# Kernel optimization log

Hardware: AMD Instinct MI355X
Metric: run time of the kernel (lower is better)

The kernel has to match this reference:

```python
import jax, jax.numpy as jnp
import numpy as np

N = 50000
E = 1600000
IN_C = 512
HID = 64
OUT_C = 64
HEADS = 2
K = 2
NEG_SLOPE = 0.2


def setup_inputs() -> dict:
    key = jax.random.key(0)
    ks = jax.random.split(key, 9)
    x = jax.random.normal(ks[0], (N, IN_C), dtype=jnp.float32)
    edge_index = jax.random.randint(ks[1], (2, E), 0, N, dtype=jnp.int64)
    edge_attr = jax.random.uniform(ks[2], (E,), dtype=jnp.float32)
    # SGConv linear (glorot-ish init)
    W_sg = jax.random.normal(ks[3], (IN_C, HID), dtype=jnp.float32) / np.sqrt(IN_C)
    b_sg = jnp.zeros((HID,), dtype=jnp.float32)
    # GATConv: lin (no bias), attention vectors, output bias (concat=False -> size OUT_C)
    W_gat = jax.random.normal(ks[4], (HID, HEADS * OUT_C), dtype=jnp.float32) / np.sqrt(HID)
    att_src = jax.random.normal(ks[5], (HEADS, OUT_C), dtype=jnp.float32) / np.sqrt(OUT_C)
    att_dst = jax.random.normal(ks[6], (HEADS, OUT_C), dtype=jnp.float32) / np.sqrt(OUT_C)
    b_gat = jnp.zeros((OUT_C,), dtype=jnp.float32)
    return {"x": x, "edge_index": edge_index, "edge_attr": edge_attr,
            "W_sg": W_sg, "b_sg": b_sg, "W_gat": W_gat,
            "att_src": att_src, "att_dst": att_dst, "b_gat": b_gat}


def reference(x, edge_index, edge_attr, W_sg, b_sg, W_gat, att_src, att_dst, b_gat):
    n = x.shape[0]
    src, dst = edge_index[0], edge_index[1]
    # add self-loops (weight 1) once; reused by SGConv (gcn_norm) and GAT
    loop = jnp.arange(n, dtype=src.dtype)
    src2 = jnp.concatenate([src, loop])
    dst2 = jnp.concatenate([dst, loop])
    ew = jnp.concatenate([edge_attr, jnp.ones((n,), x.dtype)])

    # ---- SGConv: K hops of D^-1/2 A D^-1/2, then linear ----
    deg = jax.ops.segment_sum(ew, dst2, num_segments=n)
    dinv = jnp.where(deg > 0, jax.lax.rsqrt(deg), 0.0)
    norm = dinv[src2] * ew * dinv[dst2]  # [E+N]
    h = x
    for _ in range(K):
        h = jax.ops.segment_sum(norm[:, None] * h[src2], dst2, num_segments=n)
    h = h @ W_sg + b_sg  # [N, HID]

    # activation (SELU); dropout is identity in eval mode
    h = jax.nn.selu(h)

    # ---- GATConv (heads, concat=False -> mean over heads) ----
    g = (h @ W_gat).reshape(n, HEADS, OUT_C)  # [N, H, C]
    a_src = jnp.einsum('nhc,hc->nh', g, att_src)  # [N, H]
    a_dst = jnp.einsum('nhc,hc->nh', g, att_dst)
    e = jax.nn.leaky_relu(a_src[src2] + a_dst[dst2], NEG_SLOPE)  # [E+N, H]
    # per-destination softmax (numerically stable)
    emax = jax.ops.segment_max(e, dst2, num_segments=n)
    emax = jnp.where(jnp.isfinite(emax), emax, 0.0)
    ee = jnp.exp(e - emax[dst2])
    denom = jax.ops.segment_sum(ee, dst2, num_segments=n)
    alpha = ee / jnp.maximum(denom[dst2], 1e-16)  # [E+N, H]
    out = jax.ops.segment_sum(alpha[:, :, None] * g[src2], dst2, num_segments=n)  # [N, H, C]
    return out.mean(axis=1) + b_gat  # [N, OUT_C]
```

## Files before the change

kernel.cpp:

```cpp
#include <hip/hip_runtime.h>
#include <hip/hip_fp16.h>
#include <math.h>

#define N_NODES 50000
#define N_EDGES 1600000
#define IN_CH 512
#define HID 64
#define OUTC 64
#define NEG_SLOPE 0.2f
#define EA_SCALE 131072.0f
#define PCAP 128
#define SLOTS 96

typedef __attribute__((ext_vector_type(8))) short bf16x8;
typedef __attribute__((ext_vector_type(4))) float f32x4;

__device__ __forceinline__ unsigned bf16r(float f) {
    unsigned b = __float_as_uint(f);
    return (b + 0x7FFFu + ((b >> 16) & 1u)) >> 16;
}

__device__ __forceinline__ void gload16(const void* g, void* l) {
    __builtin_amdgcn_global_load_lds(
        (const __attribute__((address_space(1))) void*)g,
        (__attribute__((address_space(3))) void*)l, 16, 0, 0);
}

__global__ void k_wsplit(const float* __restrict__ W, short* __restrict__ Wfrag) {
    int idx = blockIdx.x * 256 + threadIdx.x;
    if (idx >= IN_CH * HID) return;
    int k = idx >> 6, c = idx & 63;
    float wv = W[idx];
    unsigned h = bf16r(wv);
    float res = wv - __uint_as_float(h << 16);
    unsigned l = bf16r(res);
    int kstep = k >> 5, cb = c >> 4;
    int lane = (c & 15) | (((k >> 3) & 3) << 4);
    int j = k & 7;
    int base = ((kstep * 4 + cb) * 2) * 512 + lane * 8 + j;
    Wfrag[base] = (short)h;
    Wfrag[base + 512] = (short)l;
}

#define G1R 64
#define G1KC 64
__global__ __launch_bounds__(256) void k_gemm_hist(const float* __restrict__ x,
                                                   const short* __restrict__ Wfrag,
                                                   __half* __restrict__ p,
                                                   const int* __restrict__ src,
                                                   const int* __restrict__ dst,
                                                   const float* __restrict__ ea,
                                                   unsigned* __restrict__ deg32,
                                                   int* __restrict__ edges4) {
    __shared__ float xs[2][G1R][G1KC];
    int tid = threadIdx.x;
    int bid = blockIdx.x;

    if (bid & 1) {
        int e0 = (bid >> 1) * 2048;
        int e1 = e0 + 2048; if (e1 > N_EDGES) e1 = N_EDGES;
        for (int e = e0 + tid; e < e1; e += 256) {
            int d = dst[e];
            float w = ea[e];
            unsigned pack = (1u << 24) | (unsigned)(w * EA_SCALE);
            unsigned old = atomicAdd(&deg32[d], pack);
            int rank = (int)(old >> 24);
            if (rank < SLOTS)
                edges4[d * SLOTS + rank] =
                    (src[e] << 16) | (int)__half_as_ushort(__float2half_rn(w));
        }
        return;
    }

    int lane = tid & 63, wv = tid >> 6;
    int r0 = (bid >> 1) * G1R;
    f32x4 acc0 = {0.f, 0.f, 0.f, 0.f};
    f32x4 acc1 = {0.f, 0.f, 0.f, 0.f};
    f32x4 acc2 = {0.f, 0.f, 0.f, 0.f};
    f32x4 acc3 = {0.f, 0.f, 0.f, 0.f};

    auto stage = [&](int b, int k0) {
#pragma unroll
        for (int it = 0; it < 4; it++) {
            int rowbase = it * 16 + wv * 4;
            int row = rowbase + (lane >> 4);
            int gr = r0 + row; if (gr > N_NODES - 1) gr = N_NODES - 1;
            int col = ((lane & 15) ^ (row & 7)) << 2;
            gload16(x + (size_t)gr * IN_CH + k0 + col, &xs[b][rowbase][0]);
        }
    };

    stage(0, 0);
    asm volatile("s_waitcnt vmcnt(0)" ::: "memory");
    __syncthreads();

    int cur = 0;
    int arow = wv * 16 + (lane & 15);
    const char* xsbase = (const char*)&xs[0][0][0];
    for (int k0 = 0; k0 < IN_CH; k0 += G1KC) {
        if (k0 + G1KC < IN_CH) stage(cur ^ 1, k0 + G1KC);
#pragma unroll
        for (int kk = 0; kk < 2; kk++) {
            int ks = (k0 >> 5) + kk;
            const short* wb = Wfrag + ks * 4096 + (lane << 3);
            bf16x8 bh0 = *(const bf16x8*)(wb);
            bf16x8 bl0 = *(const bf16x8*)(wb + 512);
            bf16x8 bh1 = *(const bf16x8*)(wb + 1024);
            bf16x8 bl1 = *(const bf16x8*)(wb + 1536);
            bf16x8 bh2 = *(const bf16x8*)(wb + 2048);
            bf16x8 bl2 = *(const bf16x8*)(wb + 2560);
            bf16x8 bh3 = *(const bf16x8*)(wb + 3072);
            bf16x8 bl3 = *(const bf16x8*)(wb + 3584);
            int c16 = kk * 8 + ((lane >> 4) << 1);
            size_t rb = (size_t)cur * (G1R * G1KC * 4) + (size_t)arow * (G1KC * 4);
            float4 xa = *(const float4*)(xsbase + rb + (((c16    ) ^ (arow & 7)) << 4));
            float4 xb = *(const float4*)(xsbase + rb + (((c16 + 1) ^ (arow & 7)) << 4));
            float xv[8] = {xa.x, xa.y, xa.z, xa.w, xb.x, xb.y, xb.z, xb.w};
            bf16x8 ah, al;
#pragma unroll
            for (int j = 0; j < 8; j++) {
                unsigned b = __float_as_uint(xv[j]);
                float res = xv[j] - __uint_as_float(b & 0xFFFF0000u);
                ah[j] = (short)(b >> 16);
                al[j] = (short)(__float_as_uint(res) >> 16);
            }
            acc0 = __builtin_amdgcn_mfma_f32_16x16x32_bf16(ah, bh0, acc0, 0, 0, 0);
            acc0 = __builtin_amdgcn_mfma_f32_16x16x32_bf16(ah, bl0, acc0, 0, 0, 0);
            acc0 = __builtin_amdgcn_mfma_f32_16x16x32_bf16(al, bh0, acc0, 0, 0, 0);
            acc1 = __builtin_amdgcn_mfma_f32_16x16x32_bf16(ah, bh1, acc1, 0, 0, 0);
            acc1 = __builtin_amdgcn_mfma_f32_16x16x32_bf16(ah, bl1, acc1, 0, 0, 0);
            acc1 = __builtin_amdgcn_mfma_f32_16x16x32_bf16(al, bh1, acc1, 0, 0, 0);
            acc2 = __builtin_amdgcn_mfma_f32_16x16x32_bf16(ah, bh2, acc2, 0, 0, 0);
            acc2 = __builtin_amdgcn_mfma_f32_16x16x32_bf16(ah, bl2, acc2, 0, 0, 0);
            acc2 = __builtin_amdgcn_mfma_f32_16x16x32_bf16(al, bh2, acc2, 0, 0, 0);
            acc3 = __builtin_amdgcn_mfma_f32_16x16x32_bf16(ah, bh3, acc3, 0, 0, 0);
            acc3 = __builtin_amdgcn_mfma_f32_16x16x32_bf16(ah, bl3, acc3, 0, 0, 0);
            acc3 = __builtin_amdgcn_mfma_f32_16x16x32_bf16(al, bh3, acc3, 0, 0, 0);
        }
        asm volatile("s_waitcnt vmcnt(0)" ::: "memory");
        __syncthreads();
        cur ^= 1;
    }
    int crow = r0 + wv * 16 + ((lane >> 4) << 2);
    int ccol = lane & 15;
#pragma unroll
    for (int r = 0; r < 4; r++) {
        int gr = crow + r;
        if (gr < N_NODES) {
            p[(unsigned)gr * HID + ccol]      = __float2half(acc0[r]);
            p[(unsigned)gr * HID + 16 + ccol] = __float2half(acc1[r]);
            p[(unsigned)gr * HID + 32 + ccol] = __float2half(acc2[r]);
            p[(unsigned)gr * HID + 48 + ccol] = __float2half(acc3[r]);
        }
    }
}

__global__ void k_hscale(unsigned* __restrict__ h2, const unsigned* __restrict__ deg32,
                         float* __restrict__ dinv) {
    int idx = blockIdx.x * 256 + threadIdx.x;
    if (idx >= N_NODES * 32) return;
    int v = idx >> 5;
    float dv = rsqrtf(1.0f + (float)(deg32[v] & 0xFFFFFFu) * (1.0f / EA_SCALE));
    if ((idx & 31) == 0) dinv[v] = dv;
    unsigned u = h2[idx];
    float2 f = __half22float2(*(__half2*)&u);
    __half2 r = __floats2half2_rn(f.x * dv, f.y * dv);
    h2[idx] = *(unsigned*)&r;
}

__global__ __launch_bounds__(256) void k_hop(const uint2* __restrict__ hin4,
                                             const unsigned* __restrict__ deg32,
                                             const int* __restrict__ edges4,
                                             const float* __restrict__ dinv,
                                             uint2* __restrict__ hout4,
                                             int pw) {
    __shared__ float4 part[2][16];
    int tid = threadIdx.x;
    int w = tid >> 6, lane = tid & 63;
    int slot = w >> 1, half = w & 1;
    int cl = lane & 15, es = lane >> 4;
    int v = blockIdx.x * 2 + slot;
    int cnt = (int)(deg32[v] >> 24);
    if (cnt > SLOTS) cnt = SLOTS;
    int beg = v * SLOTS, end = beg + cnt;
    int mid = beg + (cnt >> 1);
    int lo = half ? mid : beg;
    int hi = half ? end : mid;
    float a0 = 0.f, a1 = 0.f, a2 = 0.f, a3 = 0.f;
    float b0 = 0.f, b1 = 0.f, b2 = 0.f, b3 = 0.f;
    if (!half && !es) {
        uint2 u = hin4[(unsigned)v * 16 + cl];
        float2 f0 = __half22float2(*(__half2*)&u.x);
        float2 f1 = __half22float2(*(__half2*)&u.y);
        a0 = f0.x; a1 = f0.y; a2 = f1.x; a3 = f1.y;
    }
    int i = lo;
    for (; i + 8 <= hi; i += 8) {
        int r0 = edges4[i + es];
        int r1 = edges4[i + 4 + es];
        uint2 g0 = hin4[(((unsigned)r0 >> 16) << 4) + cl];
        uint2 g1 = hin4[(((unsigned)r1 >> 16) << 4) + cl];
        float w0 = __half2float(__ushort_as_half((unsigned short)(r0 & 0xFFFF)));
        float w1 = __half2float(__ushort_as_half((unsigned short)(r1 & 0xFFFF)));
        float2 g0a = __half22float2(*(__half2*)&g0.x);
        float2 g0b = __half22float2(*(__half2*)&g0.y);
        float2 g1a = __half22float2(*(__half2*)&g1.x);
        float2 g1b = __half22float2(*(__half2*)&g1.y);
        a0 += w0 * g0a.x; a1 += w0 * g0a.y; a2 += w0 * g0b.x; a3 += w0 * g0b.y;
        b0 += w1 * g1a.x; b1 += w1 * g1a.y; b2 += w1 * g1b.x; b3 += w1 * g1b.y;
    }
    for (; i + es < hi; i += 4) {
        int r0 = edges4[i + es];
        uint2 g0 = hin4[(((unsigned)r0 >> 16) << 4) + cl];
        float w0 = __half2float(__ushort_as_half((unsigned short)(r0 & 0xFFFF)));
        float2 g0a = __half22float2(*(__half2*)&g0.x);
        float2 g0b = __half22float2(*(__half2*)&g0.y);
        a0 += w0 * g0a.x; a1 += w0 * g0a.y; a2 += w0 * g0b.x; a3 += w0 * g0b.y;
    }
    a0 += b0; a1 += b1; a2 += b2; a3 += b3;
    a0 += __shfl_xor(a0, 16); a1 += __shfl_xor(a1, 16);
    a2 += __shfl_xor(a2, 16); a3 += __shfl_xor(a3, 16);
    a0 += __shfl_xor(a0, 32); a1 += __shfl_xor(a1, 32);
    a2 += __shfl_xor(a2, 32); a3 += __shfl_xor(a3, 32);
    if (half && lane < 16) part[slot][cl] = make_float4(a0, a1, a2, a3);
    __syncthreads();
    if (!half && lane < 16) {
        float dv = dinv[v];
        float sc = (pw == 2) ? dv * dv : dv;
        float4 pp = part[slot][cl];
        __half2 h0 = __floats2half2_rn(sc * (a0 + pp.x), sc * (a1 + pp.y));
        __half2 h1 = __floats2half2_rn(sc * (a2 + pp.z), sc * (a3 + pp.w));
        hout4[(unsigned)v * 16 + cl] = make_uint2(*(unsigned*)&h0, *(unsigned*)&h1);
    }
}

#define G2_ROWS 32
__global__ __launch_bounds__(256) void k_act_gemm2(const __half* __restrict__ h2,
                                                   const float* __restrict__ bsg,
                                                   const float* __restrict__ Wg,
                                                   const float* __restrict__ att_s,
                                                   const float* __restrict__ att_d,
                                                   uint2* __restrict__ g4h,
                                                   float2* __restrict__ asrc2,
                                                   float4* __restrict__ admm) {
    __shared__ float hs[G2_ROWS][HID];
    int tid = threadIdx.x;
    int wave = tid >> 6, lane = tid & 63;
    int r0 = blockIdx.x * G2_ROWS;
    int rbase = wave * 8;

    const float SC = 1.0507009873554805f, AL = 1.6732632423543772f;
    {
        int row = tid >> 3, c0 = (tid & 7) * 8;
        int r = r0 + row;
        float vals[8];
        if (r < N_NODES) {
            uint4 raw = *(const uint4*)(h2 + (unsigned)r * HID + c0);
            float2 f0 = __half22float2(*(__half2*)&raw.x);
            float2 f1 = __half22float2(*(__half2*)&raw.y);
            float2 f2 = __half22float2(*(__half2*)&raw.z);
            float2 f3 = __half22float2(*(__half2*)&raw.w);
            vals[0] = f0.x; vals[1] = f0.y; vals[2] = f1.x; vals[3] = f1.y;
            vals[4] = f2.x; vals[5] = f2.y; vals[6] = f3.x; vals[7] = f3.y;
        } else {
#pragma unroll
            for (int j = 0; j < 8; j++) vals[j] = 0.f;
        }
#pragma unroll
        for (int j = 0; j < 8; j++) {
            float hv = vals[j] + bsg[c0 + j];
            hv = (hv > 0.f) ? SC * hv : SC * AL * (__expf(hv) - 1.f);
            hs[row][c0 + j] = hv;
        }
    }
    __syncthreads();

    float accx[8], accy[8];
#pragma unroll
    for (int j = 0; j < 8; j++) { accx[j] = 0.f; accy[j] = 0.f; }
#pragma unroll 2
    for (int k = 0; k < HID; k++) {
        float w0 = Wg[(size_t)k * 128 + lane];
        float w1 = Wg[(size_t)k * 128 + 64 + lane];
#pragma unroll
        for (int j = 0; j < 8; j++) {
            float hk = hs[rbase + j][k];
            accx[j] += hk * w0;
            accy[j] += hk * w1;
        }
    }
    float ats0 = att_s[lane], ats1 = att_s[64 + lane];
    float atd0 = att_d[lane], atd1 = att_d[64 + lane];
#pragma unroll
    for (int j = 0; j < 8; j++) {
        int v = r0 + rbase + j;
        if (v >= N_NODES) break;
        __half2 gp = __floats2half2_rn(accx[j], accy[j]);
        unsigned gpu = *(unsigned*)&gp;
        unsigned other = (unsigned)__shfl_xor((int)gpu, 1);
        if (!(lane & 1)) g4h[(unsigned)v * 32 + (lane >> 1)] = make_uint2(gpu, other);
        float s0 = accx[j] * ats0, s1 = accy[j] * ats1;
        float d0 = accx[j] * atd0, d1 = accy[j] * atd1;
#pragma unroll
        for (int o = 32; o > 0; o >>= 1) {
            s0 += __shfl_xor(s0, o);
            s1 += __shfl_xor(s1, o);
            d0 += __shfl_xor(d0, o);
            d1 += __shfl_xor(d1, o);
        }
        if (lane == 0) {
            asrc2[v] = make_float2(s0, s1);
            float m0 = s0 + d0; m0 = (m0 > 0.f) ? m0 : NEG_SLOPE * m0;
            float m1 = s1 + d1; m1 = (m1 > 0.f) ? m1 : NEG_SLOPE * m1;
            admm[v] = make_float4(d0, d1, m0, m1);
        }
    }
}

__global__ __launch_bounds__(256) void k_gat(const uint2* __restrict__ g4h,
                                             const float2* __restrict__ asrc2,
                                             const float4* __restrict__ admm,
                                             const unsigned* __restrict__ deg32,
                                             const int* __restrict__ edges4,
                                             const float* __restrict__ bgat,
                                             float* __restrict__ out) {
    __shared__ int4 pbuf[2][2][PCAP];
    __shared__ float4 pacc[2][32];
    __shared__ float2 pden[2][32];
    int tid = threadIdx.x;
    int w = tid >> 6, lane = tid & 63;
    int slot = w >> 1, half = w & 1;
    int cl = lane & 31, es = lane >> 5;
    int v = blockIdx.x * 2 + slot;
    float4 am = admm[v];
    int cnt = (int)(deg32[v] >> 24);
    if (cnt > SLOTS) cnt = SLOTS;
    int beg = v * SLOTS, end = beg + cnt;
    int mid = beg + (cnt >> 1);
    int lo = half ? mid : beg;
    int hi = half ? end : mid;
    int n = hi - lo;

    float pd0 = 0.f, pd1 = 0.f;
    for (int i = lo + lane; i < hi; i += 64) {
        int r = edges4[i];
        unsigned s = (unsigned)r >> 16;
        float2 a = asrc2[s];
        float t0 = a.x + am.x; t0 = (t0 > 0.f) ? t0 : NEG_SLOPE * t0;
        float t1 = a.y + am.y; t1 = (t1 > 0.f) ? t1 : NEG_SLOPE * t1;
        float p0 = __expf(t0 - am.z);
        float p1 = __expf(t1 - am.w);
        int idx = i - lo;
        if (idx < PCAP)
            pbuf[slot][half][idx] = make_int4((int)(s << 5), __float_as_int(p0), __float_as_int(p1), 0);
        pd0 += p0; pd1 += p1;
    }
#pragma unroll
    for (int o = 32; o > 0; o >>= 1) {
        pd0 += __shfl_xor(pd0, o);
        pd1 += __shfl_xor(pd1, o);
    }
    if (!half) { pd0 += 1.f; pd1 += 1.f; }

    float aA = 0.f, aB = 0.f, aC = 0.f, aD = 0.f;
    float bA = 0.f, bB = 0.f, bC = 0.f, bD = 0.f;
    if (!half && !es) {
        uint2 gs = g4h[(unsigned)v * 32 + cl];
        float2 gx = __half22float2(*(__half2*)&gs.x);
        float2 gy = __half22float2(*(__half2*)&gs.y);
        aA = gx.x; aB = gx.y; aC = gy.x; aD = gy.y;
    }
    int n1 = (n < PCAP) ? n : PCAP;
    int ii = 0;
    for (; ii + 8 <= n1; ii += 8) {
        int4 e0 = pbuf[slot][half][ii + es];
        int4 e1 = pbuf[slot][half][ii + 2 + es];
        int4 e2 = pbuf[slot][half][ii + 4 + es];
        int4 e3 = pbuf[slot][half][ii + 6 + es];
        uint2 g0 = g4h[(unsigned)(e0.x + cl)];
        uint2 g1 = g4h[(unsigned)(e1.x + cl)];
        uint2 g2 = g4h[(unsigned)(e2.x + cl)];
        uint2 g3 = g4h[(unsigned)(e3.x + cl)];
        float p00 = __int_as_float(e0.y), p01 = __int_as_float(e0.z);
        float p10 = __int_as_float(e1.y), p11 = __int_as_float(e1.z);
        float p20 = __int_as_float(e2.y), p21 = __int_as_float(e2.z);
        float p30 = __int_as_float(e3.y), p31 = __int_as_float(e3.z);
        float2 g0x = __half22float2(*(__half2*)&g0.x);
        float2 g0y = __half22float2(*(__half2*)&g0.y);
        float2 g1x = __half22float2(*(__half2*)&g1.x);
        float2 g1y = __half22float2(*(__half2*)&g1.y);
        float2 g2x = __half22float2(*(__half2*)&g2.x);
        float2 g2y = __half22float2(*(__half2*)&g2.y);
        float2 g3x = __half22float2(*(__half2*)&g3.x);
        float2 g3y = __half22float2(*(__half2*)&g3.y);
        aA += p00 * g0x.x; aB += p01 * g0x.y; aC += p00 * g0y.x; aD += p01 * g0y.y;
        bA += p10 * g1x.x; bB += p11 * g1x.y; bC += p10 * g1y.x; bD += p11 * g1y.y;
        aA += p20 * g2x.x; aB += p21 * g2x.y; aC += p20 * g2y.x; aD += p21 * g2y.y;
        bA += p30 * g3x.x; bB += p31 * g3x.y; bC += p30 * g3y.x; bD += p31 * g3y.y;
    }
    for (; ii + es < n1; ii += 2) {
        int4 e0 = pbuf[slot][half][ii + es];
        uint2 g0 = g4h[(unsigned)(e0.x + cl)];
        float p00 = __int_as_float(e0.y), p01 = __int_as_float(e0.z);
        float2 g0x = __half22float2(*(__half2*)&g0.x);
        float2 g0y = __half22float2(*(__half2*)&g0.y);
        aA += p00 * g0x.x; aB += p01 * g0x.y; aC += p00 * g0y.x; aD += p01 * g0y.y;
    }
    for (int jj = PCAP + es; jj < n; jj += 2) {
        int r = edges4[lo + jj];
        unsigned s = (unsigned)r >> 16;
        float2 a = asrc2[s];
        float t0 = a.x + am.x; t0 = (t0 > 0.f) ? t0 : NEG_SLOPE * t0;
        float t1 = a.y + am.y; t1 = (t1 > 0.f) ? t1 : NEG_SLOPE * t1;
        float p0 = __expf(t0 - am.z);
        float p1 = __expf(t1 - am.w);
        uint2 g0 = g4h[(s << 5) + cl];
        float2 g0x = __half22float2(*(__half2*)&g0.x);
        float2 g0y = __half22float2(*(__half2*)&g0.y);
        aA += p0 * g0x.x; aB += p1 * g0x.y; aC += p0 * g0y.x; aD += p1 * g0y.y;
    }
    aA += bA; aB += bB; aC += bC; aD += bD;
    aA += __shfl_xor(aA, 32); aB += __shfl_xor(aB, 32);
    aC += __shfl_xor(aC, 32); aD += __shfl_xor(aD, 32);
    if (half && lane < 32) {
        pacc[slot][cl] = make_float4(aA, aB, aC, aD);
        pden[slot][cl] = make_float2(pd0, pd1);
    }
    __syncthreads();
    if (!half && lane < 32) {
        float4 pa = pacc[slot][cl];
        float2 pd = pden[slot][cl];
        float r0 = 1.f / (pd0 + pd.x), r1 = 1.f / (pd1 + pd.y);
        float oe = 0.5f * ((aA + pa.x) * r0 + (aB + pa.y) * r1) + bgat[cl * 2];
        float oo = 0.5f * ((aC + pa.z) * r0 + (aD + pa.w) * r1) + bgat[cl * 2 + 1];
        *(float2*)&out[(unsigned)v * OUTC + cl * 2] = make_float2(oe, oo);
    }
}

extern "C" void kernel_launch(void* const* d_in, const int* in_sizes, int n_in,
                              void* d_out, int out_size, void* d_ws, size_t ws_size,
                              hipStream_t stream) {
    const float* x     = (const float*)d_in[0];
    const int*   ei    = (const int*)d_in[1];
    const float* ea    = (const float*)d_in[2];
    const float* Wsg   = (const float*)d_in[3];
    const float* bsg   = (const float*)d_in[4];
    const float* Wg    = (const float*)d_in[5];
    const float* att_s = (const float*)d_in[6];
    const float* att_d = (const float*)d_in[7];
    const float* bgat  = (const float*)d_in[8];
    const int* src = ei;
    const int* dst = ei + N_EDGES;
    float* out = (float*)d_out;

    char* ws = (char*)d_ws;
    size_t off = 0;
    auto alloc = [&](size_t bytes) -> void* {
        void* p = ws + off;
        off = (off + bytes + 255) & ~(size_t)255;
        return p;
    };
    unsigned* deg32  = (unsigned*)alloc((size_t)N_NODES * 4);
    float*    dinv   = (float*)alloc((size_t)N_NODES * 4);
    int*      edges4 = (int*)alloc((size_t)N_NODES * SLOTS * 4);
    short*    Wfrag  = (short*)alloc((size_t)IN_CH * HID * 2 * 2);
    __half*   h0     = (__half*)alloc((size_t)N_NODES * HID * 2);
    __half*   h1     = (__half*)alloc((size_t)N_NODES * HID * 2);
    uint2*    g4h    = (uint2*)alloc((size_t)N_NODES * 32 * 8);
    float2*   asrc2  = (float2*)alloc((size_t)N_NODES * 8);
    float4*   admm   = (float4*)alloc((size_t)N_NODES * 16);
    (void)ws_size; (void)in_sizes; (void)n_in; (void)out_size;

    hipMemsetAsync(deg32, 0, (size_t)N_NODES * 4, stream);

    k_wsplit<<<(IN_CH * HID + 255) / 256, 256, 0, stream>>>(Wsg, Wfrag);

    k_gemm_hist<<<1564, 256, 0, stream>>>(x, Wfrag, h0, src, dst, ea, deg32, edges4);

    k_hscale<<<(N_NODES * 32 + 255) / 256, 256, 0, stream>>>((unsigned*)h0, deg32, dinv);

    k_hop<<<N_NODES / 2, 256, 0, stream>>>((const uint2*)h0, deg32, edges4, dinv, (uint2*)h1, 2);
    k_hop<<<N_NODES / 2, 256, 0, stream>>>((const uint2*)h1, deg32, edges4, dinv, (uint2*)h0, 1);
    k_act_gemm2<<<(N_NODES + G2_ROWS - 1) / G2_ROWS, 256, 0, stream>>>(h0, bsg, Wg, att_s, att_d, g4h, asrc2, admm);
    k_gat<<<N_NODES / 2, 256, 0, stream>>>(g4h, asrc2, admm, deg32, edges4, bgat, out);
}
```

Baseline: 279.9 us.

## Fuse second hop with SELU+GAT linear and widen gathers to 16-byte loads

```diff
diff --git a/kernel.cpp b/kernel.cpp
--- a/kernel.cpp
+++ b/kernel.cpp
@@ -9,7 +9,7 @@
 #define OUTC 64
 #define NEG_SLOPE 0.2f
 #define EA_SCALE 131072.0f
-#define PCAP 128
+#define PCAP 64
 #define SLOTS 96
 
 typedef __attribute__((ext_vector_type(8))) short bf16x8;
@@ -24,6 +24,10 @@
     __builtin_amdgcn_global_load_lds(
         (const __attribute__((address_space(1))) void*)g,
         (__attribute__((address_space(3))) void*)l, 16, 0, 0);
+}
+
+__device__ __forceinline__ float2 h2f2(unsigned u) {
+    return __half22float2(*(__half2*)&u);
 }
 
 __global__ void k_wsplit(const float* __restrict__ W, short* __restrict__ Wfrag) {
@@ -163,22 +167,21 @@
     float dv = rsqrtf(1.0f + (float)(deg32[v] & 0xFFFFFFu) * (1.0f / EA_SCALE));
     if ((idx & 31) == 0) dinv[v] = dv;
     unsigned u = h2[idx];
-    float2 f = __half22float2(*(__half2*)&u);
+    float2 f = h2f2(u);
     __half2 r = __floats2half2_rn(f.x * dv, f.y * dv);
     h2[idx] = *(unsigned*)&r;
 }
 
-__global__ __launch_bounds__(256) void k_hop(const uint2* __restrict__ hin4,
+__global__ __launch_bounds__(256) void k_hop(const uint4* __restrict__ hin,
                                              const unsigned* __restrict__ deg32,
                                              const int* __restrict__ edges4,
                                              const float* __restrict__ dinv,
-                                             uint2* __restrict__ hout4,
-                                             int pw) {
-    __shared__ float4 part[2][16];
+                                             uint4* __restrict__ hout) {
+    __shared__ float part[2][8][8];
     int tid = threadIdx.x;
     int w = tid >> 6, lane = tid & 63;
     int slot = w >> 1, half = w & 1;
-    int cl = lane & 15, es = lane >> 4;
+    int cl = lane & 7, es = lane >> 3;
     int v = blockIdx.x * 2 + slot;
     int cnt = (int)(deg32[v] >> 24);
     if (cnt > SLOTS) cnt = SLOTS;
@@ -186,138 +189,182 @@
     int mid = beg + (cnt >> 1);
     int lo = half ? mid : beg;
     int hi = half ? end : mid;
-    float a0 = 0.f, a1 = 0.f, a2 = 0.f, a3 = 0.f;
-    float b0 = 0.f, b1 = 0.f, b2 = 0.f, b3 = 0.f;
+    float a[8], b[8];
+#pragma unroll
+    for (int j = 0; j < 8; j++) { a[j] = 0.f; b[j] = 0.f; }
     if (!half && !es) {
-        uint2 u = hin4[(unsigned)v * 16 + cl];
-        float2 f0 = __half22float2(*(__half2*)&u.x);
-        float2 f1 = __half22float2(*(__half2*)&u.y);
-        a0 = f0.x; a1 = f0.y; a2 = f1.x; a3 = f1.y;
+        uint4 u = hin[(unsigned)v * 8 + cl];
+        float2 f0 = h2f2(u.x), f1 = h2f2(u.y), f2 = h2f2(u.z), f3 = h2f2(u.w);
+        a[0] = f0.x; a[1] = f0.y; a[2] = f1.x; a[3] = f1.y;
+        a[4] = f2.x; a[5] = f2.y; a[6] = f3.x; a[7] = f3.y;
     }
     int i = lo;
-    for (; i + 8 <= hi; i += 8) {
+    for (; i + 16 <= hi; i += 16) {
         int r0 = edges4[i + es];
-        int r1 = edges4[i + 4 + es];
-        uint2 g0 = hin4[(((unsigned)r0 >> 16) << 4) + cl];
-        uint2 g1 = hin4[(((unsigned)r1 >> 16) << 4) + cl];
+        int r1 = edges4[i + 8 + es];
+        uint4 g0 = hin[(((unsigned)r0 >> 16) << 3) + cl];
+        uint4 g1 = hin[(((unsigned)r1 >> 16) << 3) + cl];
         float w0 = __half2float(__ushort_as_half((unsigned short)(r0 & 0xFFFF)));
         float w1 = __half2float(__ushort_as_half((unsigned short)(r1 & 0xFFFF)));
-        float2 g0a = __half22float2(*(__half2*)&g0.x);
-        float2 g0b = __half22float2(*(__half2*)&g0.y);
-        float2 g1a = __half22float2(*(__half2*)&g1.x);
-        float2 g1b = __half22float2(*(__half2*)&g1.y);
-        a0 += w0 * g0a.x; a1 += w0 * g0a.y; a2 += w0 * g0b.x; a3 += w0 * g0b.y;
-        b0 += w1 * g1a.x; b1 += w1 * g1a.y; b2 += w1 * g1b.x; b3 += w1 * g1b.y;
-    }
-    for (; i + es < hi; i += 4) {
+        float2 f0 = h2f2(g0.x), f1 = h2f2(g0.y), f2 = h2f2(g0.z), f3 = h2f2(g0.w);
+        float2 e0 = h2f2(g1.x), e1 = h2f2(g1.y), e2 = h2f2(g1.z), e3 = h2f2(g1.w);
+        a[0] += w0 * f0.x; a[1] += w0 * f0.y; a[2] += w0 * f1.x; a[3] += w0 * f1.y;
+        a[4] += w0 * f2.x; a[5] += w0 * f2.y; a[6] += w0 * f3.x; a[7] += w0 * f3.y;
+        b[0] += w1 * e0.x; b[1] += w1 * e0.y; b[2] += w1 * e1.x; b[3] += w1 * e1.y;
+        b[4] += w1 * e2.x; b[5] += w1 * e2.y; b[6] += w1 * e3.x; b[7] += w1 * e3.y;
+    }
+    for (; i + es < hi; i += 8) {
         int r0 = edges4[i + es];
-        uint2 g0 = hin4[(((unsigned)r0 >> 16) << 4) + cl];
+        uint4 g0 = hin[(((unsigned)r0 >> 16) << 3) + cl];
         float w0 = __half2float(__ushort_as_half((unsigned short)(r0 & 0xFFFF)));
-        float2 g0a = __half22float2(*(__half2*)&g0.x);
-        float2 g0b = __half22float2(*(__half2*)&g0.y);
-        a0 += w0 * g0a.x; a1 += w0 * g0a.y; a2 += w0 * g0b.x; a3 += w0 * g0b.y;
-    }
-    a0 += b0; a1 += b1; a2 += b2; a3 += b3;
-    a0 += __shfl_xor(a0, 16); a1 += __shfl_xor(a1, 16);
-    a2 += __shfl_xor(a2, 16); a3 += __shfl_xor(a3, 16);
-    a0 += __shfl_xor(a0, 32); a1 += __shfl_xor(a1, 32);
-    a2 += __shfl_xor(a2, 32); a3 += __shfl_xor(a3, 32);
-    if (half && lane < 16) part[slot][cl] = make_float4(a0, a1, a2, a3);
+        float2 f0 = h2f2(g0.x), f1 = h2f2(g0.y), f2 = h2f2(g0.z), f3 = h2f2(g0.w);
+        a[0] += w0 * f0.x; a[1] += w0 * f0.y; a[2] += w0 * f1.x; a[3] += w0 * f1.y;
+        a[4] += w0 * f2.x; a[5] += w0 * f2.y; a[6] += w0 * f3.x; a[7] += w0 * f3.y;
+    }
+#pragma unroll
+    for (int j = 0; j < 8; j++) {
+        a[j] += b[j];
+        a[j] += __shfl_xor(a[j], 8);
+        a[j] += __shfl_xor(a[j], 16);
+        a[j] += __shfl_xor(a[j], 32);
+    }
+    if (half && lane < 8) {
+#pragma unroll
+        for (int j = 0; j < 8; j++) part[slot][cl][j] = a[j];
+    }
     __syncthreads();
-    if (!half && lane < 16) {
+    if (!half && lane < 8) {
         float dv = dinv[v];
-        float sc = (pw == 2) ? dv * dv : dv;
-        float4 pp = part[slot][cl];
-        __half2 h0 = __floats2half2_rn(sc * (a0 + pp.x), sc * (a1 + pp.y));
-        __half2 h1 = __floats2half2_rn(sc * (a2 + pp.z), sc * (a3 + pp.w));
-        hout4[(unsigned)v * 16 + cl] = make_uint2(*(unsigned*)&h0, *(unsigned*)&h1);
-    }
-}
-
-#define G2_ROWS 32
-__global__ __launch_bounds__(256) void k_act_gemm2(const __half* __restrict__ h2,
-                                                   const float* __restrict__ bsg,
-                                                   const float* __restrict__ Wg,
-                                                   const float* __restrict__ att_s,
-                                                   const float* __restrict__ att_d,
-                                                   uint2* __restrict__ g4h,
-                                                   float2* __restrict__ asrc2,
-                                                   float4* __restrict__ admm) {
-    __shared__ float hs[G2_ROWS][HID];
+        float sc = dv * dv;
+        __half2 h0 = __floats2half2_rn(sc * (a[0] + part[slot][cl][0]), sc * (a[1] + part[slot][cl][1]));
+        __half2 h1 = __floats2half2_rn(sc * (a[2] + part[slot][cl][2]), sc * (a[3] + part[slot][cl][3]));
+        __half2 h2_ = __floats2half2_rn(sc * (a[4] + part[slot][cl][4]), sc * (a[5] + part[slot][cl][5]));
+        __half2 h3 = __floats2half2_rn(sc * (a[6] + part[slot][cl][6]), sc * (a[7] + part[slot][cl][7]));
+        hout[(unsigned)v * 8 + cl] =
+            make_uint4(*(unsigned*)&h0, *(unsigned*)&h1, *(unsigned*)&h2_, *(unsigned*)&h3);
+    }
+}
+
+__global__ __launch_bounds__(256) void k_hop2g(const uint4* __restrict__ hin,
+                                               const unsigned* __restrict__ deg32,
+                                               const int* __restrict__ edges4,
+                                               const float* __restrict__ dinv,
+                                               const float* __restrict__ bsg,
+                                               const float* __restrict__ Wg,
+                                               const float* __restrict__ att_s,
+                                               const float* __restrict__ att_d,
+                                               uint4* __restrict__ g4h,
+                                               float2* __restrict__ asrc2,
+                                               float4* __restrict__ admm) {
+    __shared__ float part[2][8][8];
+    __shared__ float hrow[2][HID];
+    __shared__ float gtmp[2][2][64];
+    __shared__ float2 sd[2][2];
     int tid = threadIdx.x;
-    int wave = tid >> 6, lane = tid & 63;
-    int r0 = blockIdx.x * G2_ROWS;
-    int rbase = wave * 8;
-
-    const float SC = 1.0507009873554805f, AL = 1.6732632423543772f;
-    {
-        int row = tid >> 3, c0 = (tid & 7) * 8;
-        int r = r0 + row;
-        float vals[8];
-        if (r < N_NODES) {
-            uint4 raw = *(const uint4*)(h2 + (unsigned)r * HID + c0);
-            float2 f0 = __half22float2(*(__half2*)&raw.x);
-            float2 f1 = __half22float2(*(__half2*)&raw.y);
-            float2 f2 = __half22float2(*(__half2*)&raw.z);
-            float2 f3 = __half22float2(*(__half2*)&raw.w);
-            vals[0] = f0.x; vals[1] = f0.y; vals[2] = f1.x; vals[3] = f1.y;
-            vals[4] = f2.x; vals[5] = f2.y; vals[6] = f3.x; vals[7] = f3.y;
-        } else {
-#pragma unroll
-            for (int j = 0; j < 8; j++) vals[j] = 0.f;
+    int w = tid >> 6, lane = tid & 63;
+    int slot = w >> 1, half = w & 1;
+    int cl = lane & 7, es = lane >> 3;
+    int v = blockIdx.x * 2 + slot;
+    int cnt = (int)(deg32[v] >> 24);
+    if (cnt > SLOTS) cnt = SLOTS;
+    int beg = v * SLOTS, end = beg + cnt;
+    int mid = beg + (cnt >> 1);
+    int lo = half ? mid : beg;
+    int hi = half ? end : mid;
+    float a[8], b[8];
+#pragma unroll
+    for (int j = 0; j < 8; j++) { a[j] = 0.f; b[j] = 0.f; }
+    if (!half && !es) {
+        uint4 u = hin[(unsigned)v * 8 + cl];
+        float2 f0 = h2f2(u.x), f1 = h2f2(u.y), f2 = h2f2(u.z), f3 = h2f2(u.w);
+        a[0] = f0.x; a[1] = f0.y; a[2] = f1.x; a[3] = f1.y;
+        a[4] = f2.x; a[5] = f2.y; a[6] = f3.x; a[7] = f3.y;
+    }
+    int i = lo;
+    for (; i + 16 <= hi; i += 16) {
+        int r0 = edges4[i + es];
+        int r1 = edges4[i + 8 + es];
+        uint4 g0 = hin[(((unsigned)r0 >> 16) << 3) + cl];
+        uint4 g1 = hin[(((unsigned)r1 >> 16) << 3) + cl];
+        float w0 = __half2float(__ushort_as_half((unsigned short)(r0 & 0xFFFF)));
+        float w1 = __half2float(__ushort_as_half((unsigned short)(r1 & 0xFFFF)));
+        float2 f0 = h2f2(g0.x), f1 = h2f2(g0.y), f2 = h2f2(g0.z), f3 = h2f2(g0.w);
+        float2 e0 = h2f2(g1.x), e1 = h2f2(g1.y), e2 = h2f2(g1.z), e3 = h2f2(g1.w);
+        a[0] += w0 * f0.x; a[1] += w0 * f0.y; a[2] += w0 * f1.x; a[3] += w0 * f1.y;
+        a[4] += w0 * f2.x; a[5] += w0 * f2.y; a[6] += w0 * f3.x; a[7] += w0 * f3.y;
+        b[0] += w1 * e0.x; b[1] += w1 * e0.y; b[2] += w1 * e1.x; b[3] += w1 * e1.y;
+        b[4] += w1 * e2.x; b[5] += w1 * e2.y; b[6] += w1 * e3.x; b[7] += w1 * e3.y;
+    }
+    for (; i + es < hi; i += 8) {
+        int r0 = edges4[i + es];
+        uint4 g0 = hin[(((unsigned)r0 >> 16) << 3) + cl];
+        float w0 = __half2float(__ushort_as_half((unsigned short)(r0 & 0xFFFF)));
+        float2 f0 = h2f2(g0.x), f1 = h2f2(g0.y), f2 = h2f2(g0.z), f3 = h2f2(g0.w);
+        a[0] += w0 * f0.x; a[1] += w0 * f0.y; a[2] += w0 * f1.x; a[3] += w0 * f1.y;
+        a[4] += w0 * f2.x; a[5] += w0 * f2.y; a[6] += w0 * f3.x; a[7] += w0 * f3.y;
+    }
+#pragma unroll
+    for (int j = 0; j < 8; j++) {
+        a[j] += b[j];
+        a[j] += __shfl_xor(a[j], 8);
+        a[j] += __shfl_xor(a[j], 16);
+        a[j] += __shfl_xor(a[j], 32);
+    }
+    if (half && lane < 8) {
+#pragma unroll
+        for (int j = 0; j < 8; j++) part[slot][cl][j] = a[j];
+    }
+    __syncthreads();
+    if (!half && lane < 8) {
+        float dv = dinv[v];
+        const float SC = 1.0507009873554805f, AL = 1.6732632423543772f;
+#pragma unroll
+        for (int j = 0; j < 8; j++) {
+            float hv = dv * (a[j] + part[slot][cl][j]) + bsg[cl * 8 + j];
+            hv = (hv > 0.f) ? SC * hv : SC * AL * (__expf(hv) - 1.f);
+            hrow[slot][cl * 8 + j] = hv;
         }
-#pragma unroll
-        for (int j = 0; j < 8; j++) {
-            float hv = vals[j] + bsg[c0 + j];
-            hv = (hv > 0.f) ? SC * hv : SC * AL * (__expf(hv) - 1.f);
-            hs[row][c0 + j] = hv;
-        }
     }
     __syncthreads();
 
-    float accx[8], accy[8];
-#pragma unroll
-    for (int j = 0; j < 8; j++) { accx[j] = 0.f; accy[j] = 0.f; }
-#pragma unroll 2
-    for (int k = 0; k < HID; k++) {
-        float w0 = Wg[(size_t)k * 128 + lane];
-        float w1 = Wg[(size_t)k * 128 + 64 + lane];
-#pragma unroll
-        for (int j = 0; j < 8; j++) {
-            float hk = hs[rbase + j][k];
-            accx[j] += hk * w0;
-            accy[j] += hk * w1;
-        }
-    }
-    float ats0 = att_s[lane], ats1 = att_s[64 + lane];
-    float atd0 = att_d[lane], atd1 = att_d[64 + lane];
-#pragma unroll
-    for (int j = 0; j < 8; j++) {
-        int v = r0 + rbase + j;
-        if (v >= N_NODES) break;
-        __half2 gp = __floats2half2_rn(accx[j], accy[j]);
-        unsigned gpu = *(unsigned*)&gp;
-        unsigned other = (unsigned)__shfl_xor((int)gpu, 1);
-        if (!(lane & 1)) g4h[(unsigned)v * 32 + (lane >> 1)] = make_uint2(gpu, other);
-        float s0 = accx[j] * ats0, s1 = accy[j] * ats1;
-        float d0 = accx[j] * atd0, d1 = accy[j] * atd1;
-#pragma unroll
-        for (int o = 32; o > 0; o >>= 1) {
-            s0 += __shfl_xor(s0, o);
-            s1 += __shfl_xor(s1, o);
-            d0 += __shfl_xor(d0, o);
-            d1 += __shfl_xor(d1, o);
-        }
-        if (lane == 0) {
-            asrc2[v] = make_float2(s0, s1);
-            float m0 = s0 + d0; m0 = (m0 > 0.f) ? m0 : NEG_SLOPE * m0;
-            float m1 = s1 + d1; m1 = (m1 > 0.f) ? m1 : NEG_SLOPE * m1;
-            admm[v] = make_float4(d0, d1, m0, m1);
-        }
-    }
-}
-
-__global__ __launch_bounds__(256) void k_gat(const uint2* __restrict__ g4h,
+    int node = slot, head = half;
+    float g = 0.f;
+    const float* wcol = Wg + head * 64 + lane;
+#pragma unroll 8
+    for (int k = 0; k < HID; k++) g += hrow[node][k] * wcol[(size_t)k * 128];
+    gtmp[node][head][lane] = g;
+    float s = g * att_s[head * 64 + lane];
+    float d = g * att_d[head * 64 + lane];
+#pragma unroll
+    for (int o = 32; o > 0; o >>= 1) {
+        s += __shfl_xor(s, o);
+        d += __shfl_xor(d, o);
+    }
+    if (lane == 0) sd[node][head] = make_float2(s, d);
+    __syncthreads();
+
+    if (tid < 32) {
+        int nd = tid >> 4, j = tid & 15;
+        const float* g0 = gtmp[nd][0];
+        const float* g1 = gtmp[nd][1];
+        __half2 p0 = __floats2half2_rn(g0[4 * j], g0[4 * j + 1]);
+        __half2 p1 = __floats2half2_rn(g0[4 * j + 2], g0[4 * j + 3]);
+        __half2 p2 = __floats2half2_rn(g1[4 * j], g1[4 * j + 1]);
+        __half2 p3 = __floats2half2_rn(g1[4 * j + 2], g1[4 * j + 3]);
+        g4h[(unsigned)(blockIdx.x * 2 + nd) * 16 + j] =
+            make_uint4(*(unsigned*)&p0, *(unsigned*)&p1, *(unsigned*)&p2, *(unsigned*)&p3);
+    } else if (tid >= 32 && tid < 34) {
+        int nd = tid - 32;
+        int vv = blockIdx.x * 2 + nd;
+        float2 h0sd = sd[nd][0], h1sd = sd[nd][1];
+        asrc2[vv] = make_float2(h0sd.x, h1sd.x);
+        float m0 = h0sd.x + h0sd.y; m0 = (m0 > 0.f) ? m0 : NEG_SLOPE * m0;
+        float m1 = h1sd.x + h1sd.y; m1 = (m1 > 0.f) ? m1 : NEG_SLOPE * m1;
+        admm[vv] = make_float4(h0sd.y, h1sd.y, m0, m1);
+    }
+}
+
+__global__ __launch_bounds__(256) void k_gat(const uint4* __restrict__ g4h,
                                              const float2* __restrict__ asrc2,
                                              const float4* __restrict__ admm,
                                              const unsigned* __restrict__ deg32,
@@ -325,12 +372,13 @@
                                              const float* __restrict__ bgat,
                                              float* __restrict__ out) {
     __shared__ int4 pbuf[2][2][PCAP];
-    __shared__ float4 pacc[2][32];
-    __shared__ float2 pden[2][32];
+    __shared__ float paccA[2][16][4];
+    __shared__ float paccB[2][16][4];
+    __shared__ float2 pdenS[2];
     int tid = threadIdx.x;
     int w = tid >> 6, lane = tid & 63;
     int slot = w >> 1, half = w & 1;
-    int cl = lane & 31, es = lane >> 5;
+    int cl = lane & 15, es = lane >> 4;
     int v = blockIdx.x * 2 + slot;
     float4 am = admm[v];
     int cnt = (int)(deg32[v] >> 24);
@@ -352,7 +400,7 @@
         float p1 = __expf(t1 - am.w);
         int idx = i - lo;
         if (idx < PCAP)
-            pbuf[slot][half][idx] = make_int4((int)(s << 5), __float_as_int(p0), __float_as_int(p1), 0);
+            pbuf[slot][half][idx] = make_int4((int)(s << 4), __float_as_int(p0), __float_as_int(p1), 0);
         pd0 += p0; pd1 += p1;
     }
 #pragma unroll
@@ -361,79 +409,67 @@
         pd1 += __shfl_xor(pd1, o);
     }
     if (!half) { pd0 += 1.f; pd1 += 1.f; }
-
-    float aA = 0.f, aB = 0.f, aC = 0.f, aD = 0.f;
-    float bA = 0.f, bB = 0.f, bC = 0.f, bD = 0.f;
+    if (half && lane == 0) pdenS[slot] = make_float2(pd0, pd1);
+
+    float A0 = 0.f, A1 = 0.f, A2 = 0.f, A3 = 0.f;
+    float B0 = 0.f, B1 = 0.f, B2 = 0.f, B3 = 0.f;
+    float C0 = 0.f, C1 = 0.f, C2 = 0.f, C3 = 0.f;
+    float D0 = 0.f, D1 = 0.f, D2 = 0.f, D3 = 0.f;
     if (!half && !es) {
-        uint2 gs = g4h[(unsigned)v * 32 + cl];
-        float2 gx = __half22float2(*(__half2*)&gs.x);
-        float2 gy = __half22float2(*(__half2*)&gs.y);
-        aA = gx.x; aB = gx.y; aC = gy.x; aD = gy.y;
-    }
-    int n1 = (n < PCAP) ? n : PCAP;
+        uint4 gs = g4h[(unsigned)v * 16 + cl];
+        float2 gx = h2f2(gs.x), gy = h2f2(gs.y), gz = h2f2(gs.z), gw = h2f2(gs.w);
+        A0 = gx.x; A1 = gx.y; A2 = gy.x; A3 = gy.y;
+        B0 = gz.x; B1 = gz.y; B2 = gw.x; B3 = gw.y;
+    }
     int ii = 0;
-    for (; ii + 8 <= n1; ii += 8) {
+    for (; ii + 8 <= n; ii += 8) {
         int4 e0 = pbuf[slot][half][ii + es];
-        int4 e1 = pbuf[slot][half][ii + 2 + es];
-        int4 e2 = pbuf[slot][half][ii + 4 + es];
-        int4 e3 = pbuf[slot][half][ii + 6 + es];
-        uint2 g0 = g4h[(unsigned)(e0.x + cl)];
-        uint2 g1 = g4h[(unsigned)(e1.x + cl)];
-        uint2 g2 = g4h[(unsigned)(e2.x + cl)];
-        uint2 g3 = g4h[(unsigned)(e3.x + cl)];
+        int4 e1 = pbuf[slot][half][ii + 4 + es];
+        uint4 g0 = g4h[(unsigned)(e0.x + cl)];
+        uint4 g1 = g4h[(unsigned)(e1.x + cl)];
         float p00 = __int_as_float(e0.y), p01 = __int_as_float(e0.z);
         float p10 = __int_as_float(e1.y), p11 = __int_as_float(e1.z);
-        float p20 = __int_as_float(e2.y), p21 = __int_as_float(e2.z);
-        float p30 = __int_as_float(e3.y), p31 = __int_as_float(e3.z);
-        float2 g0x = __half22float2(*(__half2*)&g0.x);
-        float2 g0y = __half22float2(*(__half2*)&g0.y);
-        float2 g1x = __half22float2(*(__half2*)&g1.x);
-        float2 g1y = __half22float2(*(__half2*)&g1.y);
-        float2 g2x = __half22float2(*(__half2*)&g2.x);
-        float2 g2y = __half22float2(*(__half2*)&g2.y);
-        float2 g3x = __half22float2(*(__half2*)&g3.x);
-        float2 g3y = __half22float2(*(__half2*)&g3.y);
-        aA += p00 * g0x.x; aB += p01 * g0x.y; aC += p00 * g0y.x; aD += p01 * g0y.y;
-        bA += p10 * g1x.x; bB += p11 * g1x.y; bC += p10 * g1y.x; bD += p11 * g1y.y;
-        aA += p20 * g2x.x; aB += p21 * g2x.y; aC += p20 * g2y.x; aD += p21 * g2y.y;
-        bA += p30 * g3x.x; bB += p31 * g3x.y; bC += p30 * g3y.x; bD += p31 * g3y.y;
-    }
-    for (; ii + es < n1; ii += 2) {
+        float2 gx = h2f2(g0.x), gy = h2f2(g0.y), gz = h2f2(g0.z), gw = h2f2(g0.w);
+        float2 hx = h2f2(g1.x), hy = h2f2(g1.y), hz = h2f2(g1.z), hw = h2f2(g1.w);
+        A0 += p00 * gx.x; A1 += p00 * gx.y; A2 += p00 * gy.x; A3 += p00 * gy.y;
+        B0 += p01 * gz.x; B1 += p01 * gz.y; B2 += p01 * gw.x; B3 += p01 * gw.y;
+        C0 += p10 * hx.x; C1 += p10 * hx.y; C2 += p10 * hy.x; C3 += p10 * hy.y;
+        D0 += p11 * hz.x; D1 += p11 * hz.y; D2 += p11 * hw.x; D3 += p11 * hw.y;
+    }
+    for (; ii + es < n; ii += 4) {
         int4 e0 = pbuf[slot][half][ii + es];
-        uint2 g0 = g4h[(unsigned)(e0.x + cl)];
+        uint4 g0 = g4h[(unsigned)(e0.x + cl)];
         float p00 = __int_as_float(e0.y), p01 = __int_as_float(e0.z);
-        float2 g0x = __half22float2(*(__half2*)&g0.x);
-        float2 g0y = __half22float2(*(__half2*)&g0.y);
-        aA += p00 * g0x.x; aB += p01 * g0x.y; aC += p00 * g0y.x; aD += p01 * g0y.y;
-    }
-    for (int jj = PCAP + es; jj < n; jj += 2) {
-        int r = edges4[lo + jj];
-        unsigned s = (unsigned)r >> 16;
-        float2 a = asrc2[s];
-        float t0 = a.x + am.x; t0 = (t0 > 0.f) ? t0 : NEG_SLOPE * t0;
-        float t1 = a.y + am.y; t1 = (t1 > 0.f) ? t1 : NEG_SLOPE * t1;
-        float p0 = __expf(t0 - am.z);
-        float p1 = __expf(t1 - am.w);
-        uint2 g0 = g4h[(s << 5) + cl];
-        float2 g0x = __half22float2(*(__half2*)&g0.x);
-        float2 g0y = __half22float2(*(__half2*)&g0.y);
-        aA += p0 * g0x.x; aB += p1 * g0x.y; aC += p0 * g0y.x; aD += p1 * g0y.y;
-    }
-    aA += bA; aB += bB; aC += bC; aD += bD;
-    aA += __shfl_xor(aA, 32); aB += __shfl_xor(aB, 32);
-    aC += __shfl_xor(aC, 32); aD += __shfl_xor(aD, 32);
-    if (half && lane < 32) {
-        pacc[slot][cl] = make_float4(aA, aB, aC, aD);
-        pden[slot][cl] = make_float2(pd0, pd1);
+        float2 gx = h2f2(g0.x), gy = h2f2(g0.y), gz = h2f2(g0.z), gw = h2f2(g0.w);
+        A0 += p00 * gx.x; A1 += p00 * gx.y; A2 += p00 * gy.x; A3 += p00 * gy.y;
+        B0 += p01 * gz.x; B1 += p01 * gz.y; B2 += p01 * gw.x; B3 += p01 * gw.y;
+    }
+    A0 += C0; A1 += C1; A2 += C2; A3 += C3;
+    B0 += D0; B1 += D1; B2 += D2; B3 += D3;
+    A0 += __shfl_xor(A0, 16); A1 += __shfl_xor(A1, 16);
+    A2 += __shfl_xor(A2, 16); A3 += __shfl_xor(A3, 16);
+    B0 += __shfl_xor(B0, 16); B1 += __shfl_xor(B1, 16);
+    B2 += __shfl_xor(B2, 16); B3 += __shfl_xor(B3, 16);
+    A0 += __shfl_xor(A0, 32); A1 += __shfl_xor(A1, 32);
+    A2 += __shfl_xor(A2, 32); A3 += __shfl_xor(A3, 32);
+    B0 += __shfl_xor(B0, 32); B1 += __shfl_xor(B1, 32);
+    B2 += __shfl_xor(B2, 32); B3 += __shfl_xor(B3, 32);
+    if (half && lane < 16) {
+        paccA[slot][cl][0] = A0; paccA[slot][cl][1] = A1;
+        paccA[slot][cl][2] = A2; paccA[slot][cl][3] = A3;
+        paccB[slot][cl][0] = B0; paccB[slot][cl][1] = B1;
+        paccB[slot][cl][2] = B2; paccB[slot][cl][3] = B3;
     }
     __syncthreads();
-    if (!half && lane < 32) {
-        float4 pa = pacc[slot][cl];
-        float2 pd = pden[slot][cl];
-        float r0 = 1.f / (pd0 + pd.x), r1 = 1.f / (pd1 + pd.y);
-        float oe = 0.5f * ((aA + pa.x) * r0 + (aB + pa.y) * r1) + bgat[cl * 2];
-        float oo = 0.5f * ((aC + pa.z) * r0 + (aD + pa.w) * r1) + bgat[cl * 2 + 1];
-        *(float2*)&out[(unsigned)v * OUTC + cl * 2] = make_float2(oe, oo);
+    if (!half && lane < 16) {
+        float2 pdo = pdenS[slot];
+        float r0 = 1.f / (pd0 + pdo.x), r1 = 1.f / (pd1 + pdo.y);
+        float4 o4;
+        o4.x = 0.5f * ((A0 + paccA[slot][cl][0]) * r0 + (B0 + paccB[slot][cl][0]) * r1) + bgat[cl * 4 + 0];
+        o4.y = 0.5f * ((A1 + paccA[slot][cl][1]) * r0 + (B1 + paccB[slot][cl][1]) * r1) + bgat[cl * 4 + 1];
+        o4.z = 0.5f * ((A2 + paccA[slot][cl][2]) * r0 + (B2 + paccB[slot][cl][2]) * r1) + bgat[cl * 4 + 2];
+        o4.w = 0.5f * ((A3 + paccA[slot][cl][3]) * r0 + (B3 + paccB[slot][cl][3]) * r1) + bgat[cl * 4 + 3];
+        *(float4*)&out[(unsigned)v * OUTC + cl * 4] = o4;
     }
 }
 
@@ -466,7 +502,7 @@
     short*    Wfrag  = (short*)alloc((size_t)IN_CH * HID * 2 * 2);
     __half*   h0     = (__half*)alloc((size_t)N_NODES * HID * 2);
     __half*   h1     = (__half*)alloc((size_t)N_NODES * HID * 2);
-    uint2*    g4h    = (uint2*)alloc((size_t)N_NODES * 32 * 8);
+    uint4*    g4h    = (uint4*)alloc((size_t)N_NODES * 16 * 16);
     float2*   asrc2  = (float2*)alloc((size_t)N_NODES * 8);
     float4*   admm   = (float4*)alloc((size_t)N_NODES * 16);
     (void)ws_size; (void)in_sizes; (void)n_in; (void)out_size;
@@ -479,8 +515,8 @@
 
     k_hscale<<<(N_NODES * 32 + 255) / 256, 256, 0, stream>>>((unsigned*)h0, deg32, dinv);
 
-    k_hop<<<N_NODES / 2, 256, 0, stream>>>((const uint2*)h0, deg32, edges4, dinv, (uint2*)h1, 2);
-    k_hop<<<N_NODES / 2, 256, 0, stream>>>((const uint2*)h1, deg32, edges4, dinv, (uint2*)h0, 1);
-    k_act_gemm2<<<(N_NODES + G2_ROWS - 1) / G2_ROWS, 256, 0, stream>>>(h0, bsg, Wg, att_s, att_d, g4h, asrc2, admm);
+    k_hop<<<N_NODES / 2, 256, 0, stream>>>((const uint4*)h0, deg32, edges4, dinv, (uint4*)h1);
+    k_hop2g<<<N_NODES / 2, 256, 0, stream>>>((const uint4*)h1, deg32, edges4, dinv,
+                                             bsg, Wg, att_s, att_d, g4h, asrc2, admm);
     k_gat<<<N_NODES / 2, 256, 0, stream>>>(g4h, asrc2, admm, deg32, edges4, bgat, out);
 }
```

Result: slower. 297.9 us (+6.4%).
